# Kernel optimization log

Hardware: AMD Instinct MI355X
Metric: run time of the kernel (lower is better)

The kernel has to match this reference:

```python
import jax, jax.numpy as jnp
import numpy as np

B, C1, C2, D, NH, H, W = 2, 64, 256, 256, 8, 64, 64
HD = D // NH
EPS = 1e-5


def setup_inputs() -> dict:
    key = jax.random.key(0)
    ks = jax.random.split(key, 12)
    s = lambda fan_in: 1.0 / np.sqrt(fan_in)
    return {
        "F_lidar": jax.random.normal(ks[0], (B, C1, H, W), jnp.float32),
        "F_cam": jax.random.normal(ks[1], (B, C2, H, W), jnp.float32),
        "Wq": jax.random.normal(ks[2], (D, C1), jnp.float32) * s(C1),
        "Wk": jax.random.normal(ks[3], (D, C2), jnp.float32) * s(C2),
        "Wv": jax.random.normal(ks[4], (D, C2), jnp.float32) * s(C2),
        "Wo": jax.random.normal(ks[5], (D, D), jnp.float32) * s(D),
        "Wres": jax.random.normal(ks[6], (D, C1), jnp.float32) * s(C1),
        "g1": jnp.ones((D,), jnp.float32),
        "b1": jnp.zeros((D,), jnp.float32),
        "g2": jnp.ones((D,), jnp.float32),
        "b2": jnp.zeros((D,), jnp.float32),
        "W1": jax.random.normal(ks[7], (4 * D, D), jnp.float32) * s(D),
        "bf1": jnp.zeros((4 * D,), jnp.float32),
        "W2": jax.random.normal(ks[8], (D, 4 * D), jnp.float32) * s(4 * D),
        "bf2": jnp.zeros((D,), jnp.float32),
    }


def _layernorm(x, g, b):
    mu = jnp.mean(x, axis=-1, keepdims=True)
    var = jnp.mean(jnp.square(x - mu), axis=-1, keepdims=True)
    return (x - mu) * jax.lax.rsqrt(var + EPS) * g + b


def reference(F_lidar, F_cam, Wq, Wk, Wv, Wo, Wres, g1, b1, g2, b2, W1, bf1, W2, bf2):
    b, _, h, w = F_lidar.shape
    n = h * w
    # channels-last token views: (B, HW, C)
    xl = F_lidar.reshape(b, C1, n).transpose(0, 2, 1)
    xc = F_cam.reshape(b, C2, n).transpose(0, 2, 1)
    # 1x1 conv projections == per-token matmuls
    Q = jnp.einsum('bnc,dc->bnd', xl, Wq).reshape(b, n, NH, HD).transpose(0, 2, 1, 3)
    K = jnp.einsum('bnc,dc->bnd', xc, Wk).reshape(b, n, NH, HD).transpose(0, 2, 1, 3)
    V = jnp.einsum('bnc,dc->bnd', xc, Wv).reshape(b, n, NH, HD).transpose(0, 2, 1, 3)
    scale = HD ** -0.5
    scores = jnp.einsum('bhqd,bhkd->bhqk', Q, K) * scale  # (B,NH,HW,HW)
    attn = jax.nn.softmax(scores, axis=-1)
    out = jnp.einsum('bhqk,bhkd->bhqd', attn, V)
    out = out.transpose(0, 2, 1, 3).reshape(b, n, D)
    out = jnp.einsum('bnd,ed->bne', out, Wo)
    resid = jnp.einsum('bnc,dc->bnd', xl, Wres)
    x = _layernorm(resid + out, g1, b1)
    # FFN (dropout = identity in eval)
    hdn = jax.nn.relu(jnp.einsum('bnd,fd->bnf', x, W1) + bf1)
    ffn = jnp.einsum('bnf,df->bnd', hdn, W2) + bf2
    x = _layernorm(x + ffn, g2, b2)
    return x.transpose(0, 2, 1).reshape(b, D, h, w)
```

## Files before the change

### kernel.cpp

```cpp
#include <hip/hip_runtime.h>
#include <hip/hip_bf16.h>
#include <math.h>

#define NB 2
#define C1 64
#define C2 256
#define DD 256
#define NHH 8
#define HDD 32
#define NN 4096
#define FF 1024
#define MTOT (NB*NN)
#define KVB 128

typedef unsigned short u16;
typedef __attribute__((ext_vector_type(8))) short bf16x8;
typedef __attribute__((ext_vector_type(4))) float f32x4;
typedef __attribute__((ext_vector_type(4))) unsigned short us4;
typedef __attribute__((ext_vector_type(4))) unsigned int u32x4;

__device__ __forceinline__ u16 f2bf(float f) {
    union { float f; unsigned int i; } u; u.f = f;
    unsigned int r = u.i + 0x7FFFu + ((u.i >> 16) & 1u);
    return (u16)(r >> 16);
}

__device__ __forceinline__ unsigned cvt_pk_bf16(float a, float b) {
    unsigned r; asm("v_cvt_pk_bf16_f32 %0, %1, %2" : "=v"(r) : "v"(a), "v"(b)); return r;
}

__device__ __forceinline__ void glds16(const void* g, void* l) {
    __builtin_amdgcn_global_load_lds(
        (__attribute__((address_space(1))) void*)g,
        (__attribute__((address_space(3))) void*)l, 16, 0, 0);
}

__global__ __launch_bounds__(256) void wconv(
    const float* __restrict__ Wq, const float* __restrict__ Wres,
    const float* __restrict__ Wk, const float* __restrict__ Wv,
    const float* __restrict__ Wo, const float* __restrict__ W1,
    const float* __restrict__ W2, u16* __restrict__ d)
{
    int i = blockIdx.x * 256 + threadIdx.x;
    if (i >= 753664) return;
    const float* s; int off;
    if      (i <  16384) { s = Wq;   off = i; }
    else if (i <  32768) { s = Wres; off = i -  16384; }
    else if (i <  98304) { s = Wk;   off = i -  32768; }
    else if (i < 163840) { s = Wv;   off = i -  98304; }
    else if (i < 229376) { s = Wo;   off = i - 163840; }
    else if (i < 491520) { s = W1;   off = i - 229376; }
    else                 { s = W2;   off = i - 491520; }
    d[i] = f2bf(s[off]);
}

__global__ __launch_bounds__(256) void tconv(const float* __restrict__ src,
                                             u16* __restrict__ dst, int C)
{
    __shared__ float tile[64][65];
    const int n0 = blockIdx.x * 64;
    const int c0 = blockIdx.y * 64;
    const int b  = blockIdx.z;
    const int t  = threadIdx.x;
#pragma unroll
    for (int i = 0; i < 4; ++i) {
        int cc = t + i * 256;
        int c = cc >> 4, off = (cc & 15) * 4;
        const float4 v = *(const float4*)&src[((size_t)b*C + c0 + c)*NN + n0 + off];
        tile[c][off+0] = v.x; tile[c][off+1] = v.y;
        tile[c][off+2] = v.z; tile[c][off+3] = v.w;
    }
    __syncthreads();
    const int n = t >> 2, cch = (t & 3) * 16;
    bf16x8 t0, t1;
#pragma unroll
    for (int i = 0; i < 8; ++i) ((u16*)&t0)[i] = f2bf(tile[cch + i][n]);
#pragma unroll
    for (int i = 0; i < 8; ++i) ((u16*)&t1)[i] = f2bf(tile[cch + 8 + i][n]);
    u16* dp = &dst[((size_t)b*NN + n0 + n)*C + c0 + cch];
    *(bf16x8*)&dp[0] = t0;
    *(bf16x8*)&dp[8] = t1;
}

template<int MODE>
__global__ __launch_bounds__(256) void gemm_bt(
    const u16* __restrict__ A, const u16* __restrict__ Bw,
    int M, int N, int K,
    const float* __restrict__ bias, const float* __restrict__ add,
    float* __restrict__ outf, u16* __restrict__ outb, float scale)
{
    __shared__ u16 lA[128*32];
    __shared__ u16 lB[128*32];
    const int bm = blockIdx.x * 128;
    const int bn = blockIdx.y * 128;
    const int t = threadIdx.x, lane = t & 63, wid = t >> 6;
    const int wr = (wid >> 1) * 64, wc = (wid & 1) * 64;
    const int lrow = lane & 15, lk = (lane >> 4) * 8;
    const int srow = wid*32 + (lane >> 2);
    const int soff = (lane & 3) * 8;
    const u16* aS = &A[(size_t)(bm + srow)*K + soff];
    const u16* bS = &Bw[(size_t)(bn + srow)*K + soff];
    u16* aL = &lA[wid*1024];
    u16* bL = &lB[wid*1024];
    f32x4 acc[4][4] = {};
    for (int k0 = 0; k0 < K; k0 += 32) {
        glds16(aS + k0,                  aL);
        glds16(aS + (size_t)16*K + k0,   aL + 512);
        glds16(bS + k0,                  bL);
        glds16(bS + (size_t)16*K + k0,   bL + 512);
        __syncthreads();
        bf16x8 af[4], bfr[4];
#pragma unroll
        for (int mf = 0; mf < 4; ++mf)
            af[mf] = *(const bf16x8*)&lA[(wr + mf*16 + lrow)*32 + lk];
#pragma unroll
        for (int nf = 0; nf < 4; ++nf)
            bfr[nf] = *(const bf16x8*)&lB[(wc + nf*16 + lrow)*32 + lk];
#pragma unroll
        for (int mf = 0; mf < 4; ++mf)
#pragma unroll
            for (int nf = 0; nf < 4; ++nf)
                acc[mf][nf] = __builtin_amdgcn_mfma_f32_16x16x32_bf16(af[mf], bfr[nf], acc[mf][nf], 0, 0, 0);
        __syncthreads();
    }
#pragma unroll
    for (int mf = 0; mf < 4; ++mf) {
#pragma unroll
        for (int nf = 0; nf < 4; ++nf) {
#pragma unroll
            for (int j = 0; j < 4; ++j) {
                int row = bm + wr + mf*16 + (lane >> 4)*4 + j;
                int col = bn + wc + nf*16 + lrow;
                float v = acc[mf][nf][j];
                if (MODE == 0) {
                    size_t idx = (size_t)row*N + col;
                    outf[idx] = v + add[idx];
                } else if (MODE == 1) {
                    float r = v + bias[col];
                    outb[(size_t)row*N + col] = f2bf(r > 0.f ? r : 0.f);
                } else if (MODE == 2) {
                    size_t idx = (size_t)row*N + col;
                    outf[idx] = v + bias[col] + add[idx];
                } else if (MODE == 3) {
                    int b = row >> 12, n = row & 4095;
                    if (col < 256) {
                        int h = col >> 5, hd = col & 31;
                        int bh = b*NHH + h;
                        size_t idx = (((size_t)bh*256 + (n >> 4))*64
                                      + (hd >> 3)*16 + (n & 15))*8 + (hd & 7);
                        outb[idx] = f2bf(v);
                    } else {
                        int c = col - 256;
                        int h = c >> 5, hd = c & 31;
                        int hf = hd >> 4, d = hd & 15;
                        int bh = b*NHH + h;
                        int kb = n >> 5, kwb = n & 31;
                        int hp = kwb >> 4, gg = (kwb >> 2) & 3, r = kwb & 3;
                        size_t idx = ((((size_t)bh*128 + kb)*2 + hf)*64 + gg*16 + d)*8
                                   + hp*4 + r;
                        ((u16*)outf)[idx] = f2bf(v);
                    }
                } else {
                    int b = row >> 12, n = row & 4095;
                    if (col < 256) {
                        int h = col >> 5, hd = col & 31;
                        outb[(((size_t)b*NHH + h)*NN + n)*HDD + hd] = f2bf(v * scale);
                    } else {
                        outf[(size_t)row*DD + (col - 256)] = v;
                    }
                }
            }
        }
    }
}

__global__ __launch_bounds__(256) void flash_attn(
    const u16* __restrict__ Qp, const u16* __restrict__ Kperm,
    const u16* __restrict__ Vperm, u16* __restrict__ Op)
{
    __shared__ u16 Kl[2][4096];
    __shared__ u16 Vl[2][4096];
    const int id = blockIdx.x;
    const int sw = (id & 7) * 128 + (id >> 3);
    const int qt = sw & 63;
    const int bh = sw >> 6;
    const size_t base = (size_t)bh * NN * HDD;
    const int t = threadIdx.x, lane = t & 63, w = t >> 6;
    const int q0 = qt * 64;
    const int lrow = lane & 15, g = lane >> 4;

    const bf16x8 qf = *(const bf16x8*)&Qp[base + (size_t)(q0 + w*16 + lrow)*HDD + g*8];

    const u16* kgw = &Kperm[(size_t)bh*131072 + w*1024 + lane*8];
    const u16* vgw = &Vperm[(size_t)bh*131072 + w*1024 + lane*8];
    const int lw = w * 1024;

    u32x4 onesw = {0x3F803F80u, 0x3F803F80u, 0x3F803F80u, 0x3F803F80u};
    const bf16x8 ones = *(bf16x8*)&onesw;

    glds16(kgw,       &Kl[0][lw]);
    glds16(kgw + 512, &Kl[0][lw + 512]);
    glds16(vgw,       &Vl[0][lw]);
    glds16(vgw + 512, &Vl[0][lw + 512]);

    f32x4 o[2] = {};
    f32x4 osum = {};
    __syncthreads();

#define FLASH_STEP(CUR, TT)                                                    \
    {                                                                          \
        if ((TT) < 31) {                                                       \
            const u16* kg = kgw + (size_t)((TT)+1)*4096;                       \
            const u16* vg = vgw + (size_t)((TT)+1)*4096;                       \
            glds16(kg,       &Kl[(CUR)^1][lw]);                                \
            glds16(kg + 512, &Kl[(CUR)^1][lw + 512]);                          \
            glds16(vg,       &Vl[(CUR)^1][lw]);                                \
            glds16(vg + 512, &Vl[(CUR)^1][lw + 512]);                          \
        }                                                                      \
        f32x4 s[8];                                                            \
        _Pragma("unroll")                                                      \
        for (int nf = 0; nf < 8; ++nf) {                                       \
            bf16x8 kf = *(const bf16x8*)&Kl[(CUR)][nf*512 + lane*8];           \
            f32x4 z = {};                                                      \
            s[nf] = __builtin_amdgcn_mfma_f32_16x16x32_bf16(kf, qf, z, 0, 0, 0); \
        }                                                                      \
        _Pragma("unroll")                                                      \
        for (int kk = 0; kk < 4; ++kk) {                                       \
            float p0[4], p1[4];                                                \
            _Pragma("unroll")                                                  \
            for (int jj = 0; jj < 4; ++jj) {                                   \
                p0[jj] = __builtin_amdgcn_exp2f(s[2*kk][jj]);                  \
                p1[jj] = __builtin_amdgcn_exp2f(s[2*kk+1][jj]);                 \
            }                                                                  \
            u32x4 paw;                                                         \
            paw[0] = cvt_pk_bf16(p0[0], p0[1]);                                \
            paw[1] = cvt_pk_bf16(p0[2], p0[3]);                                \
            paw[2] = cvt_pk_bf16(p1[0], p1[1]);                                \
            paw[3] = cvt_pk_bf16(p1[2], p1[3]);                                \
            bf16x8 pa = *(bf16x8*)&paw;                                        \
            _Pragma("unroll")                                                  \
            for (int hf = 0; hf < 2; ++hf) {                                   \
                bf16x8 vf = *(const bf16x8*)&Vl[(CUR)][kk*1024 + hf*512 + lane*8]; \
                o[hf] = __builtin_amdgcn_mfma_f32_16x16x32_bf16(pa, vf, o[hf], 0, 0, 0); \
            }                                                                  \
            osum = __builtin_amdgcn_mfma_f32_16x16x32_bf16(pa, ones, osum, 0, 0, 0); \
        }                                                                      \
        __syncthreads();                                                       \
    }

    for (int tt = 0; tt < 32; tt += 2) {
        FLASH_STEP(0, tt)
        FLASH_STEP(1, tt + 1)
    }
#undef FLASH_STEP

    const int b = bh >> 3, h = bh & 7;
#pragma unroll
    for (int hf = 0; hf < 2; ++hf)
#pragma unroll
        for (int r = 0; r < 4; ++r) {
            int q = q0 + w*16 + g*4 + r;
            int d = h*HDD + hf*16 + lrow;
            Op[((size_t)b*NN + q)*DD + d] = f2bf(o[hf][r] / osum[r]);
        }
}

__global__ __launch_bounds__(256) void ln_fuse(const float* __restrict__ y,
    const float* __restrict__ g, const float* __restrict__ be,
    float* __restrict__ x, u16* __restrict__ xb)
{
    const int row = blockIdx.x * 4 + (threadIdx.x >> 6);
    const int lane = threadIdx.x & 63;
    const float4 v = *(const float4*)&y[(size_t)row*DD + lane*4];
    float s1 = v.x + v.y + v.z + v.w;
    float s2 = v.x*v.x + v.y*v.y + v.z*v.z + v.w*v.w;
#pragma unroll
    for (int m = 1; m <= 32; m <<= 1) { s1 += __shfl_xor(s1, m); s2 += __shfl_xor(s2, m); }
    float mean = s1 * (1.f/DD);
    float var  = s2 * (1.f/DD) - mean*mean;
    float rstd = rsqrtf(var + 1e-5f);
    const float vv[4] = {v.x, v.y, v.z, v.w};
    float4 xo; us4 xo16;
#pragma unroll
    for (int i = 0; i < 4; ++i) {
        int d = lane*4 + i;
        float r = (vv[i] - mean) * rstd * g[d] + be[d];
        ((float*)&xo)[i] = r;
        xo16[i] = f2bf(r);
    }
    *(float4*)&x[(size_t)row*DD + lane*4] = xo;
    *(us4*)&xb[(size_t)row*DD + lane*4] = xo16;
}

__global__ __launch_bounds__(256) void ln2_transpose(const float* __restrict__ z,
    const float* __restrict__ g, const float* __restrict__ be,
    float* __restrict__ out)
{
    __shared__ float tile[32][257];
    const int n0 = blockIdx.x * 32;
    const int b = blockIdx.y;
    const int t = threadIdx.x, lane = t & 63, w = t >> 6;
    for (int r8 = 0; r8 < 8; ++r8) {
        int r = w*8 + r8;
        const float4 v = *(const float4*)&z[((size_t)b*NN + n0 + r)*DD + lane*4];
        float s1 = v.x + v.y + v.z + v.w;
        float s2 = v.x*v.x + v.y*v.y + v.z*v.z + v.w*v.w;
#pragma unroll
        for (int m = 1; m <= 32; m <<= 1) { s1 += __shfl_xor(s1, m); s2 += __shfl_xor(s2, m); }
        float mean = s1 * (1.f/DD);
        float var  = s2 * (1.f/DD) - mean*mean;
        float rstd = rsqrtf(var + 1e-5f);
        const float vv[4] = {v.x, v.y, v.z, v.w};
#pragma unroll
        for (int i = 0; i < 4; ++i) {
            int d = lane*4 + i;
            tile[r][d] = (vv[i] - mean)*rstd*g[d] + be[d];
        }
    }
    __syncthreads();
    const int n = t & 31, dg = t >> 5;
    for (int dd = 0; dd < 32; ++dd) {
        int d = dd*8 + dg;
        out[((size_t)b*DD + d)*NN + n0 + n] = tile[n][d];
    }
}

extern "C" void kernel_launch(void* const* d_in, const int* in_sizes, int n_in,
                              void* d_out, int out_size, void* d_ws, size_t ws_size,
                              hipStream_t stream)
{
    const float* F_lidar = (const float*)d_in[0];
    const float* F_cam   = (const float*)d_in[1];
    const float* Wq  = (const float*)d_in[2];
    const float* Wk  = (const float*)d_in[3];
    const float* Wv  = (const float*)d_in[4];
    const float* Wo  = (const float*)d_in[5];
    const float* Wrs = (const float*)d_in[6];
    const float* g1  = (const float*)d_in[7];
    const float* b1  = (const float*)d_in[8];
    const float* g2  = (const float*)d_in[9];
    const float* b2  = (const float*)d_in[10];
    const float* W1  = (const float*)d_in[11];
    const float* bf1 = (const float*)d_in[12];
    const float* W2  = (const float*)d_in[13];
    const float* bf2 = (const float*)d_in[14];
    float* out = (float*)d_out;

    char* ws = (char*)d_ws;
    size_t cur = 0;
    auto carve = [&](size_t bytes) {
        size_t o = cur; cur += (bytes + 255) & ~(size_t)255; return (void*)(ws + o);
    };
    u16* wb    = (u16*)carve(753664u * 2);
    u16* xl    = (u16*)carve((size_t)MTOT * C1 * 2);
    u16* xc    = (u16*)carve((size_t)MTOT * C2 * 2);
    u16* Qb    = (u16*)carve((size_t)MTOT * DD * 2);
    u16* Kperm = (u16*)carve((size_t)MTOT * DD * 2);
    u16* Vperm = (u16*)carve((size_t)MTOT * DD * 2);
    float* resid = (float*)carve((size_t)MTOT * DD * 4);
    u16* attn  = (u16*)carve((size_t)MTOT * DD * 2);
    float* y   = (float*)carve((size_t)MTOT * DD * 4);
    float* x   = (float*)carve((size_t)MTOT * DD * 4);
    u16* xb    = (u16*)carve((size_t)MTOT * DD * 2);
    u16* hdn   = (u16*)carve((size_t)MTOT * FF * 2);
    float* zb  = y;

    u16* WqRes = wb;
    u16* WkWv  = wb + 32768;
    u16* Wob   = wb + 163840;
    u16* W1b   = wb + 229376;
    u16* W2b   = wb + 491520;

    wconv<<<2944, 256, 0, stream>>>(Wq, Wrs, Wk, Wv, Wo, W1, W2, wb);
    tconv<<<dim3(64, 1, NB), 256, 0, stream>>>(F_lidar, xl, C1);
    tconv<<<dim3(64, 4, NB), 256, 0, stream>>>(F_cam, xc, C2);

    const float qscale = 1.4426950408889634f / sqrtf((float)HDD);
    gemm_bt<4><<<dim3(64, 4), 256, 0, stream>>>(xl, WqRes, MTOT, 512, C1,
        nullptr, nullptr, resid, Qb, qscale);
    gemm_bt<3><<<dim3(64, 4), 256, 0, stream>>>(xc, WkWv, MTOT, 512, C2,
        nullptr, nullptr, (float*)Vperm, Kperm, 1.f);

    flash_attn<<<1024, 256, 0, stream>>>(Qb, Kperm, Vperm, attn);

    gemm_bt<0><<<dim3(64, 2), 256, 0, stream>>>(attn, Wob, MTOT, DD, DD,
        nullptr, resid, y, nullptr, 1.f);
    ln_fuse<<<2048, 256, 0, stream>>>(y, g1, b1, x, xb);
    gemm_bt<1><<<dim3(64, 8), 256, 0, stream>>>(xb, W1b, MTOT, FF, DD,
        bf1, nullptr, nullptr, hdn, 1.f);
    gemm_bt<2><<<dim3(64, 2), 256, 0, stream>>>(hdn, W2b, MTOT, DD, FF,
        bf2, x, zb, nullptr, 1.f);
    ln2_transpose<<<dim3(128, NB), 256, 0, stream>>>(zb, g2, b2, out);
}
```

Measured before the change: 145.7 us.

## Double-buffer GEMM LDS tiles and raise wave priority around attention MFMAs

```diff
diff --git a/kernel.cpp b/kernel.cpp
--- a/kernel.cpp
+++ b/kernel.cpp
@@ -89,8 +89,8 @@
     const float* __restrict__ bias, const float* __restrict__ add,
     float* __restrict__ outf, u16* __restrict__ outb, float scale)
 {
-    __shared__ u16 lA[128*32];
-    __shared__ u16 lB[128*32];
+    __shared__ u16 lA[2][4096];
+    __shared__ u16 lB[2][4096];
     const int bm = blockIdx.x * 128;
     const int bn = blockIdx.y * 128;
     const int t = threadIdx.x, lane = t & 63, wid = t >> 6;
@@ -100,22 +100,32 @@
     const int soff = (lane & 3) * 8;
     const u16* aS = &A[(size_t)(bm + srow)*K + soff];
     const u16* bS = &Bw[(size_t)(bn + srow)*K + soff];
-    u16* aL = &lA[wid*1024];
-    u16* bL = &lB[wid*1024];
+    const int lw = wid * 1024;
     f32x4 acc[4][4] = {};
-    for (int k0 = 0; k0 < K; k0 += 32) {
-        glds16(aS + k0,                  aL);
-        glds16(aS + (size_t)16*K + k0,   aL + 512);
-        glds16(bS + k0,                  bL);
-        glds16(bS + (size_t)16*K + k0,   bL + 512);
-        __syncthreads();
+
+    glds16(aS,                  &lA[0][lw]);
+    glds16(aS + (size_t)16*K,   &lA[0][lw + 512]);
+    glds16(bS,                  &lB[0][lw]);
+    glds16(bS + (size_t)16*K,   &lB[0][lw + 512]);
+    __syncthreads();
+
+    const int nst = K >> 5;
+    for (int st = 0; st < nst; ++st) {
+        const int cur = st & 1;
+        if (st < nst - 1) {
+            const int k0 = (st + 1) * 32;
+            glds16(aS + k0,                  &lA[cur^1][lw]);
+            glds16(aS + (size_t)16*K + k0,   &lA[cur^1][lw + 512]);
+            glds16(bS + k0,                  &lB[cur^1][lw]);
+            glds16(bS + (size_t)16*K + k0,   &lB[cur^1][lw + 512]);
+        }
         bf16x8 af[4], bfr[4];
 #pragma unroll
         for (int mf = 0; mf < 4; ++mf)
-            af[mf] = *(const bf16x8*)&lA[(wr + mf*16 + lrow)*32 + lk];
+            af[mf] = *(const bf16x8*)&lA[cur][(wr + mf*16 + lrow)*32 + lk];
 #pragma unroll
         for (int nf = 0; nf < 4; ++nf)
-            bfr[nf] = *(const bf16x8*)&lB[(wc + nf*16 + lrow)*32 + lk];
+            bfr[nf] = *(const bf16x8*)&lB[cur][(wc + nf*16 + lrow)*32 + lk];
 #pragma unroll
         for (int mf = 0; mf < 4; ++mf)
 #pragma unroll
@@ -218,12 +228,14 @@
             glds16(vg + 512, &Vl[(CUR)^1][lw + 512]);                          \
         }                                                                      \
         f32x4 s[8];                                                            \
+        __builtin_amdgcn_s_setprio(1);                                         \
         _Pragma("unroll")                                                      \
         for (int nf = 0; nf < 8; ++nf) {                                       \
             bf16x8 kf = *(const bf16x8*)&Kl[(CUR)][nf*512 + lane*8];           \
             f32x4 z = {};                                                      \
             s[nf] = __builtin_amdgcn_mfma_f32_16x16x32_bf16(kf, qf, z, 0, 0, 0); \
         }                                                                      \
+        __builtin_amdgcn_s_setprio(0);                                         \
         _Pragma("unroll")                                                      \
         for (int kk = 0; kk < 4; ++kk) {                                       \
             float p0[4], p1[4];                                                \
@@ -238,12 +250,14 @@
             paw[2] = cvt_pk_bf16(p1[0], p1[1]);                                \
             paw[3] = cvt_pk_bf16(p1[2], p1[3]);                                \
             bf16x8 pa = *(bf16x8*)&paw;                                        \
+            __builtin_amdgcn_s_setprio(1);                                     \
             _Pragma("unroll")                                                  \
             for (int hf = 0; hf < 2; ++hf) {                                   \
                 bf16x8 vf = *(const bf16x8*)&Vl[(CUR)][kk*1024 + hf*512 + lane*8]; \
                 o[hf] = __builtin_amdgcn_mfma_f32_16x16x32_bf16(pa, vf, o[hf], 0, 0, 0); \
             }                                                                  \
             osum = __builtin_amdgcn_mfma_f32_16x16x32_bf16(pa, ones, osum, 0, 0, 0); \
+            __builtin_amdgcn_s_setprio(0);                                     \
         }                                                                      \
         __syncthreads();                                                       \
     }
```

Measured after the change: 141.2 us. 1.03x faster.
